# Performance work log

Hardware: AMD Instinct MI355X
Metric: run time of the kernel (lower is better)

Reference implementation:

```python
import jax, jax.numpy as jnp
import numpy as np

B, C, H, W = 32, 64, 56, 56
REPN, NK, SMALL = 50, 17, 3   # repN=64-int(64*0.23), nk=ceil(51/3)
GROUPS = 4                     # N_rep
EPS = 1e-5


def _build_index_mats():
    """Reduce the fallback's python scatter-add loops to exact linear maps.
    For flat position p=r*NK+j the roll shifts depend only on p%3, so each
    shift class s gets a (REPN,NK) count matrix over source nk-slots."""
    rng = np.random.RandomState(123)
    ghost = np.sort(rng.choice(C, C - REPN, replace=False))
    rep = np.array(sorted(set(range(C)) - set(ghost.tolist())), np.int32)
    Mh = np.zeros((3, REPN, NK), np.int32)
    Mv = np.zeros((3, REPN, NK), np.int32)
    Mid = np.zeros((REPN, NK), np.int32)
    for _ in range(GROUPS):
        for r in range(REPN):
            perm = rng.permutation(NK)
            for p in range(NK):
                Mh[(r * NK + p) % 3, r, perm[p]] += 1
        for r in range(REPN):
            perm = rng.permutation(NK)
            for p in range(NK):
                Mv[(r * NK + p) % 3, r, perm[p]] += 1
        kk = rng.randint(0, NK, REPN)
        for r in range(REPN):
            Mid[r, kk[r]] += 1
    return ghost.astype(np.int32), rep, Mh, Mv, Mid


def setup_inputs() -> dict:
    key = jax.random.key(0)
    k1, k2, k3 = jax.random.split(key, 3)
    ghost, rep, Mh, Mv, Mid = _build_index_mats()
    return {
        "inputs": jax.random.normal(k1, (B, C, H, W), jnp.float32),
        "w0": jax.random.normal(k2, (REPN * NK, 1, SMALL, SMALL), jnp.float32) * 0.1,
        "w1": jax.random.normal(k3, (REPN * NK, 1, SMALL, SMALL), jnp.float32) * 0.1,
        "Mh": jnp.asarray(Mh), "Mv": jnp.asarray(Mv), "Mid": jnp.asarray(Mid),
        "ghost_idx": jnp.asarray(ghost), "rep_idx": jnp.asarray(rep),
    }


def _bn(x):
    # BatchNorm2d in training mode, affine weight=1 / bias=0 (init values)
    m = x.mean(axis=(0, 2, 3), keepdims=True)
    v = x.var(axis=(0, 2, 3), keepdims=True)
    return (x - m) / jnp.sqrt(v + EPS)


def reference(inputs, w0, w1, Mh, Mv, Mid, ghost_idx, rep_idx):
    rep_in = inputs[:, rep_idx]      # (B, REPN, H, W)
    ghost_in = inputs[:, ghost_idx]  # (B, ghostN, H, W)

    def conv(w):  # depthwise-grouped conv: groups=REPN, each 1->NK channels
        return jax.lax.conv_general_dilated(
            rep_in, w, window_strides=(1, 1), padding=((2, 2), (2, 2)),
            dimension_numbers=('NCHW', 'OIHW', 'NCHW'),
            feature_group_count=REPN)

    out = conv(w0) + conv(w1)                       # (B, REPN*NK, H+2, W+2)
    xv = out.reshape(B, REPN, NK, H + 2, W + 2)

    Mhf, Mvf, Midf = (m.astype(xv.dtype) for m in (Mh, Mv, Mid))
    sh1, sw1 = (0, 1, 2), (0, 2, 1)   # lora1: shifts (i%3, 2i%3)
    sh2, sw2 = (0, 2, 1), (0, 1, 2)   # lora2: shifts (2i%3, i%3)

    lora1 = sum(jnp.roll(jnp.einsum('rk,brkhw->brhw', Mhf[s], xv),
                         (sh1[s], sw1[s]), axis=(2, 3)) for s in range(3))
    lora2 = sum(jnp.roll(jnp.einsum('rk,brkhw->brhw', Mvf[s], xv),
                         (sh2[s], sw2[s]), axis=(2, 3)) for s in range(3))
    small = jnp.einsum('rk,brkhw->brhw', Midf, xv)

    # center-crop back to (H, W): dh = dw = 1
    lora1 = lora1[:, :, 1:1 + H, 1:1 + W]
    lora2 = lora2[:, :, 1:1 + H, 1:1 + W]
    small = small[:, :, 1:1 + H, 1:1 + W]

    x = _bn(lora1) + _bn(lora2) + _bn(small) + rep_in
    return jnp.concatenate([x, ghost_in], axis=1)   # (B, C, H, W)
```

## Files before the change

kernel.cpp:

```cpp
#include <hip/hip_runtime.h>

#define Bn 32
#define Cn 64
#define Hn 56
#define Wn 56
#define REPN 50
#define NKn 17
#define HWn (Hn*Wn)
#define NSTATf 100352.0f
#define EPSf 1e-5f

#define GCNT_OFF 0
#define GSUM_OFF 1600
#define INIT_BYTES 8000
#define PART_OFF 4096

#define SEGH 7
#define NTASK 112
#define GRID_FUSED 1024

__device__ __forceinline__ void block_weff(int r, int tid,
        const float* __restrict__ w0, const float* __restrict__ w1,
        const int* __restrict__ Mh, const int* __restrict__ Mv,
        const int* __restrict__ Mid, float* __restrict__ swk)
{
    if (tid >= 0 && tid < 63) {
        int t = tid / 9, ij = tid - t*9;
        const int* M = (t < 3) ? (Mh + (t*REPN + r)*NKn)
                     : (t < 6) ? (Mv + ((t-3)*REPN + r)*NKn)
                               : (Mid + r*NKn);
        float acc = 0.f;
        #pragma unroll
        for (int k = 0; k < NKn; ++k)
            acc += (float)M[k] * (w0[(r*NKn + k)*9 + ij] + w1[(r*NKn + k)*9 + ij]);
        swk[t*9 + ij] = acc;
    }
}

__device__ __forceinline__ void load_row8c(const float* __restrict__ ch, int row, int q,
                                           float* __restrict__ X, float& c55)
{
    bool rv = (row >= 0) && (row < Hn);
    int rc = rv ? row : 0;
    const float* rp = ch + rc*Wn;
    float4 c0 = *(const float4*)(rp + (q ? 4*q - 4 : 0));
    float4 c1 = *(const float4*)(rp + 4*q);
    int ox = (4*q + 4 <= 55) ? 4*q + 4 : 55;
    float cx = rp[ox];
    float mr = rv ? 1.f : 0.f;
    float m0 = (rv && q > 0)  ? 1.f : 0.f;
    float mx = (rv && q < 13) ? 1.f : 0.f;
    X[0]=c0.y*m0; X[1]=c0.z*m0; X[2]=c0.w*m0;
    X[3]=c1.x*mr; X[4]=c1.y*mr; X[5]=c1.z*mr; X[6]=c1.w*mr;
    X[7]=cx*mx;
    c55 = (q == 0) ? rp[55]*mr : 0.f;
}

template <typename F>
__device__ __forceinline__ void conv_walk3(const float* __restrict__ ch,
        const float (&wk)[63], int tid, F emit)
{
    if (tid >= NTASK) return;
    int seg = tid / 14;
    int q   = tid - seg*14;
    int h0  = seg * SEGH;
    bool top = (seg == 0);

    float W[6][8], C[6], T[8];
    {
        float dummy;
        if (top) load_row8c(ch, 55, q, T, dummy);
    }
    #pragma unroll
    for (int k = 0; k < 6; ++k)
        load_row8c(ch, h0 - 3 + k, q, W[k], C[k]);

    #pragma unroll
    for (int s = 0; s < SEGH; ++s) {
        int h = h0 + s;
        float Wn8[8], Cn1;
        load_row8c(ch, h + 3, q, Wn8, Cn1);

        float l1[4], l2[4], sm[4];
        #pragma unroll
        for (int p = 0; p < 4; ++p) { l1[p]=0.f; l2[p]=0.f; sm[p]=0.f; }
        #pragma unroll
        for (int i = 0; i < 3; ++i)
            #pragma unroll
            for (int j = 0; j < 3; ++j) {
                int ij = i*3 + j;
                float wh0 = wk[ij],    wh1 = wk[9+ij],  wh2 = wk[18+ij];
                float wv0 = wk[27+ij], wv1 = wk[36+ij], wv2 = wk[45+ij];
                float wid = wk[54+ij];
                #pragma unroll
                for (int p = 0; p < 4; ++p) {
                    float a  = W[2+i][p+2+j];
                    l1[p] = fmaf(a, wh0, l1[p]);
                    l2[p] = fmaf(a, wv0, l2[p]);
                    sm[p] = fmaf(a, wid, sm[p]);
                    float bA = W[1+i][p+j];
                    l1[p] = fmaf(bA, wh1, l1[p]);
                    l2[p] = fmaf(bA, wv2, l2[p]);
                    float bB = W[i][p+1+j];
                    l1[p] = fmaf(bB, wh2, l1[p]);
                    l2[p] = fmaf(bB, wv1, l2[p]);
                }
            }
        if (q == 0) {
            #pragma unroll
            for (int i = 0; i < 3; ++i) {
                l1[0] = fmaf(C[1+i], wk[9+3*i],  l1[0]);
                l2[0] = fmaf(C[1+i], wk[45+3*i], l2[0]);
            }
        }
        if (s == 0 && top) {
            #pragma unroll
            for (int j = 0; j < 3; ++j)
                #pragma unroll
                for (int p = 0; p < 4; ++p) {
                    l1[p] = fmaf(T[p+1+j], wk[18+j], l1[p]);
                    l2[p] = fmaf(T[p+1+j], wk[36+j], l2[p]);
                }
        }
        float res[4] = {W[3][3], W[3][4], W[3][5], W[3][6]};
        emit(h, q, l1, l2, sm, res);

        #pragma unroll
        for (int k = 0; k < 5; ++k) {
            #pragma unroll
            for (int x = 0; x < 8; ++x) W[k][x] = W[k+1][x];
            C[k] = C[k+1];
        }
        #pragma unroll
        for (int x = 0; x < 8; ++x) W[5][x] = Wn8[x];
        C[5] = Cn1;
    }
}

__device__ __forceinline__ void conv_walk1(const float* __restrict__ ch,
        const float (&cw0)[9], const float (&cwA)[9], const float (&cwB)[9],
        float Kc, int tid, float* __restrict__ dst)
{
    if (tid >= NTASK) return;
    int seg = tid / 14;
    int q   = tid - seg*14;
    int h0  = seg * SEGH;
    bool top = (seg == 0);

    float W[6][8], C[6], T[8];
    {
        float dummy;
        if (top) load_row8c(ch, 55, q, T, dummy);
    }
    #pragma unroll
    for (int k = 0; k < 6; ++k)
        load_row8c(ch, h0 - 3 + k, q, W[k], C[k]);

    #pragma unroll
    for (int s = 0; s < SEGH; ++s) {
        int h = h0 + s;
        float Wn8[8], Cn1;
        load_row8c(ch, h + 3, q, Wn8, Cn1);

        float acc[4];
        #pragma unroll
        for (int p = 0; p < 4; ++p) acc[p] = 0.f;
        #pragma unroll
        for (int i = 0; i < 3; ++i)
            #pragma unroll
            for (int j = 0; j < 3; ++j) {
                int ij = i*3 + j;
                float w0c = cw0[ij], wAc = cwA[ij], wBc = cwB[ij];
                #pragma unroll
                for (int p = 0; p < 4; ++p) {
                    acc[p] = fmaf(W[2+i][p+2+j], w0c, acc[p]);
                    acc[p] = fmaf(W[1+i][p+j],   wAc, acc[p]);
                    acc[p] = fmaf(W[i][p+1+j],   wBc, acc[p]);
                }
            }
        if (q == 0) {
            #pragma unroll
            for (int i = 0; i < 3; ++i)
                acc[0] = fmaf(C[1+i], cwA[3*i], acc[0]);
        }
        if (s == 0 && top) {
            #pragma unroll
            for (int j = 0; j < 3; ++j)
                #pragma unroll
                for (int p = 0; p < 4; ++p)
                    acc[p] = fmaf(T[p+1+j], cwB[j], acc[p]);
        }
        float4 o;
        o.x = acc[0] - Kc + W[3][3];
        o.y = acc[1] - Kc + W[3][4];
        o.z = acc[2] - Kc + W[3][5];
        o.w = acc[3] - Kc + W[3][6];
        *(float4*)(dst + h*Wn + 4*q) = o;

        #pragma unroll
        for (int k = 0; k < 5; ++k) {
            #pragma unroll
            for (int x = 0; x < 8; ++x) W[k][x] = W[k+1][x];
            C[k] = C[k+1];
        }
        #pragma unroll
        for (int x = 0; x < 8; ++x) W[5][x] = Wn8[x];
        C[5] = Cn1;
    }
}

__device__ __forceinline__ void stats_and_arrive(const float* __restrict__ ch,
        const float* __restrict__ swk, int r, int tid,
        float* __restrict__ ws, float (*red)[6])
{
    float wk[63];
    #pragma unroll
    for (int i = 0; i < 63; ++i) wk[i] = swk[i];

    float s1=0.f,q1=0.f,s2=0.f,q2=0.f,s3=0.f,q3=0.f;
    conv_walk3(ch, wk, tid,
        [&](int h, int q, float* l1, float* l2, float* sm, float* res) {
            (void)h; (void)q; (void)res;
            #pragma unroll
            for (int p = 0; p < 4; ++p) {
                s1 += l1[p]; q1 += l1[p]*l1[p];
                s2 += l2[p]; q2 += l2[p]*l2[p];
                s3 += sm[p]; q3 += sm[p]*sm[p];
            }
        });
    {
        float vals[6] = {s1,q1,s2,q2,s3,q3};
        int lane = tid & 63, wave = tid >> 6;
        #pragma unroll
        for (int x = 0; x < 6; ++x) {
            float y = vals[x];
            for (int o = 32; o; o >>= 1) y += __shfl_down(y, o, 64);
            if (lane == 0) red[wave][x] = y;
        }
    }
    __syncthreads();
    if (tid < 6) {
        atomicAdd(ws + GSUM_OFF + r*8 + tid, red[0][tid] + red[1][tid]);
        __threadfence();
    }
    __syncthreads();
    if (tid == 0)
        atomicAdd(((unsigned*)ws) + GCNT_OFF + r*32, 1u);
    __syncthreads();
}

__device__ __forceinline__ void wait_and_finalize(const float* __restrict__ ch,
        const float* __restrict__ swk, int r, int tid,
        float* __restrict__ ws, float* __restrict__ sred,
        float* __restrict__ dst)
{
    if (tid == 0) {
        unsigned* gc = ((unsigned*)ws) + GCNT_OFF + r*32;
        while (atomicAdd(gc, 0u) < (unsigned)Bn)
            __builtin_amdgcn_s_sleep(8);
    }
    __syncthreads();
    if (tid < 6) sred[tid] = atomicAdd(ws + GSUM_OFF + r*8 + tid, 0.f);
    __syncthreads();

    const float inv = 1.0f / NSTATf;
    float m1 = sred[0]*inv, v1 = sred[1]*inv - m1*m1;
    float m2 = sred[2]*inv, v2 = sred[3]*inv - m2*m2;
    float m3 = sred[4]*inv, v3 = sred[5]*inv - m3*m3;
    float r1 = rsqrtf(v1 + EPSf), r2 = rsqrtf(v2 + EPSf), r3 = rsqrtf(v3 + EPSf);
    float Kc = m1*r1 + m2*r2 + m3*r3;

    float cw0[9], cwA[9], cwB[9];
    #pragma unroll
    for (int ij = 0; ij < 9; ++ij) {
        cw0[ij] = r1*swk[ij]    + r2*swk[27+ij] + r3*swk[54+ij];
        cwA[ij] = r1*swk[9+ij]  + r2*swk[45+ij];
        cwB[ij] = r1*swk[18+ij] + r2*swk[36+ij];
    }
    conv_walk1(ch, cw0, cwA, cwB, Kc, tid, dst);
}

__global__ void __launch_bounds__(128) k_fused(const float* __restrict__ in,
        const float* __restrict__ w0, const float* __restrict__ w1,
        const int* __restrict__ Mh, const int* __restrict__ Mv,
        const int* __restrict__ Mid,
        const int* __restrict__ rep_idx, const int* __restrict__ ghost_idx,
        float* __restrict__ ws, float* __restrict__ out)
{
    int tid = threadIdx.x;
    int bid = blockIdx.x;
    int b   = bid >> 5;
    int pr  = bid & 31;
    int cA  = 2*pr, cB = 2*pr + 1;

    if (pr >= REPN/2) {
        #pragma unroll
        for (int it = 0; it < 2; ++it) {
            int c = cA + it;
            int cin = ghost_idx[c - REPN];
            const float4* s4 = (const float4*)(in + ((size_t)(b*Cn + cin))*HWn);
            float4* d4 = (float4*)(out + ((size_t)(b*Cn + c))*HWn);
            for (int i = tid; i < HWn/4; i += 128) d4[i] = s4[i];
        }
        return;
    }

    __shared__ float swkA[63], swkB[63];
    __shared__ float red[2][6];
    __shared__ float sredA[6], sredB[6];

    block_weff(cA, tid,      w0, w1, Mh, Mv, Mid, swkA);
    block_weff(cB, tid - 64, w0, w1, Mh, Mv, Mid, swkB);
    __syncthreads();

    const float* chA = in + ((size_t)(b*Cn + rep_idx[cA]))*HWn;
    const float* chB = in + ((size_t)(b*Cn + rep_idx[cB]))*HWn;

    stats_and_arrive(chA, swkA, cA, tid, ws, red);
    stats_and_arrive(chB, swkB, cB, tid, ws, red);

    float* dstA = out + ((size_t)(b*Cn + cA))*HWn;
    float* dstB = out + ((size_t)(b*Cn + cB))*HWn;
    wait_and_finalize(chA, swkA, cA, tid, ws, sredA, dstA);
    wait_and_finalize(chB, swkB, cB, tid, ws, sredB, dstB);
}

__global__ void __launch_bounds__(128) k_pass1(const float* __restrict__ in,
        const float* __restrict__ w0, const float* __restrict__ w1,
        const int* __restrict__ Mh, const int* __restrict__ Mv,
        const int* __restrict__ Mid,
        const int* __restrict__ rep_idx, float* __restrict__ ws)
{
    int bid = blockIdx.x;
    int r = bid % REPN;
    int b = bid / REPN;
    int tid = threadIdx.x;

    __shared__ float swk[63];
    __shared__ float red[2][6];

    block_weff(r, tid, w0, w1, Mh, Mv, Mid, swk);
    __syncthreads();
    float wk[63];
    #pragma unroll
    for (int i = 0; i < 63; ++i) wk[i] = swk[i];

    const float* ch = in + ((size_t)(b*Cn + rep_idx[r]))*HWn;

    float s1=0.f,q1=0.f,s2=0.f,q2=0.f,s3=0.f,q3=0.f;
    conv_walk3(ch, wk, tid,
        [&](int h, int q, float* l1, float* l2, float* sm, float* res) {
            (void)h; (void)q; (void)res;
            #pragma unroll
            for (int p = 0; p < 4; ++p) {
                s1 += l1[p]; q1 += l1[p]*l1[p];
                s2 += l2[p]; q2 += l2[p]*l2[p];
                s3 += sm[p]; q3 += sm[p]*sm[p];
            }
        });

    float vals[6] = {s1,q1,s2,q2,s3,q3};
    int lane = tid & 63, wave = tid >> 6;
    #pragma unroll
    for (int x = 0; x < 6; ++x) {
        float y = vals[x];
        for (int o = 32; o; o >>= 1) y += __shfl_down(y, o, 64);
        if (lane == 0) red[wave][x] = y;
    }
    __syncthreads();
    if (tid < 6)
        ws[PART_OFF + (tid*REPN + r)*Bn + b] = red[0][tid] + red[1][tid];
}

__global__ void __launch_bounds__(128) k_pass2(const float* __restrict__ in,
        const float* __restrict__ w0, const float* __restrict__ w1,
        const int* __restrict__ Mh, const int* __restrict__ Mv,
        const int* __restrict__ Mid,
        const int* __restrict__ rep_idx, const int* __restrict__ ghost_idx,
        const float* __restrict__ ws, float* __restrict__ out)
{
    int bid = blockIdx.x;
    int c = bid & 63;
    int b = bid >> 6;
    int tid = threadIdx.x;

    if (c >= REPN) {
        int cin = ghost_idx[c - REPN];
        const float4* s4 = (const float4*)(in + ((size_t)(b*Cn + cin))*HWn);
        float4* d4 = (float4*)(out + ((size_t)(b*Cn + c))*HWn);
        for (int i = tid; i < HWn/4; i += 128) d4[i] = s4[i];
        return;
    }
    int r = c;

    __shared__ float swk[63];
    __shared__ float sred[6];

    block_weff(r, tid, w0, w1, Mh, Mv, Mid, swk);
    if (tid >= 64 && tid < 70) {
        int x = tid - 64;
        const float* pp = ws + PART_OFF + (x*REPN + r)*Bn;
        float s = 0.f;
        #pragma unroll
        for (int i = 0; i < Bn; ++i) s += pp[i];
        sred[x] = s;
    }
    __syncthreads();

    const float inv = 1.0f / NSTATf;
    float m1 = sred[0]*inv, v1 = sred[1]*inv - m1*m1;
    float m2 = sred[2]*inv, v2 = sred[3]*inv - m2*m2;
    float m3 = sred[4]*inv, v3 = sred[5]*inv - m3*m3;
    float r1 = rsqrtf(v1 + EPSf), r2 = rsqrtf(v2 + EPSf), r3 = rsqrtf(v3 + EPSf);
    float Kc = m1*r1 + m2*r2 + m3*r3;

    float cw0[9], cwA[9], cwB[9];
    #pragma unroll
    for (int ij = 0; ij < 9; ++ij) {
        cw0[ij] = r1*swk[ij]    + r2*swk[27+ij] + r3*swk[54+ij];
        cwA[ij] = r1*swk[9+ij]  + r2*swk[45+ij];
        cwB[ij] = r1*swk[18+ij] + r2*swk[36+ij];
    }

    const float* ch = in + ((size_t)(b*Cn + rep_idx[r]))*HWn;
    float* dst = out + ((size_t)(b*Cn + c))*HWn;
    conv_walk1(ch, cw0, cwA, cwB, Kc, tid, dst);
}

extern "C" void kernel_launch(void* const* d_in, const int* in_sizes, int n_in,
                              void* d_out, int out_size, void* d_ws, size_t ws_size,
                              hipStream_t stream) {
    const float* in   = (const float*)d_in[0];
    const float* w0   = (const float*)d_in[1];
    const float* w1   = (const float*)d_in[2];
    const int*   Mh   = (const int*)d_in[3];
    const int*   Mv   = (const int*)d_in[4];
    const int*   Mid  = (const int*)d_in[5];
    const int*   ghost= (const int*)d_in[6];
    const int*   rep  = (const int*)d_in[7];
    float* out  = (float*)d_out;
    float* ws   = (float*)d_ws;

    int maxBlk = 0;
    hipError_t qerr = hipOccupancyMaxActiveBlocksPerMultiprocessor(
        &maxBlk, (const void*)k_fused, 128, 0);
    bool fused_ok = (qerr == hipSuccess) && (maxBlk >= 4);

    if (fused_ok) {
        hipError_t merr = hipMemsetAsync(ws, 0, INIT_BYTES, stream);
        if (merr == hipSuccess) {
            k_fused<<<GRID_FUSED, 128, 0, stream>>>(in, w0, w1, Mh, Mv, Mid,
                                                    rep, ghost, ws, out);
            return;
        }
    }
    k_pass1<<<REPN*Bn, 128, 0, stream>>>(in, w0, w1, Mh, Mv, Mid, rep, ws);
    k_pass2<<<Bn*Cn,   128, 0, stream>>>(in, w0, w1, Mh, Mv, Mid, rep, ghost, ws, out);
}
```

Before: 118.3 us.

## Cache conv branch outputs as bf16 in LDS instead of recomputing in finalize

During the statistics pass, each block now packs the three pre-normalization branch outputs (lora1, lora2, small) into bf16 planes in shared memory. After the grid-wide statistics wait, the finalize step reads these planes and applies the per-branch BN scales plus the residual, instead of rerunning the 3x3 convolution walk. This removes the second convolution pass over the input at the cost of about 37 KB of LDS per block, which may lower occupancy. Storing the intermediates in bf16 also introduces rounding error in the normalized outputs.

Result: no change. 118.3 us (+0.1%).

```diff
diff --git a/kernel.cpp b/kernel.cpp
--- a/kernel.cpp
+++ b/kernel.cpp
@@ -18,6 +18,18 @@
 #define SEGH 7
 #define NTASK 112
 #define GRID_FUSED 1024
+#define PLW (HWn/2)
+
+__device__ __forceinline__ unsigned bfpack2(float a, float b)
+{
+    unsigned ua = __float_as_uint(a);
+    unsigned ub = __float_as_uint(b);
+    ua += 0x7FFFu + ((ua >> 16) & 1u);
+    ub += 0x7FFFu + ((ub >> 16) & 1u);
+    return (ua >> 16) | (ub & 0xFFFF0000u);
+}
+__device__ __forceinline__ float bflo(unsigned u){ return __uint_as_float(u << 16); }
+__device__ __forceinline__ float bfhi(unsigned u){ return __uint_as_float(u & 0xFFFF0000u); }
 
 __device__ __forceinline__ void block_weff(int r, int tid,
         const float* __restrict__ w0, const float* __restrict__ w1,
@@ -211,7 +223,7 @@
 
 __device__ __forceinline__ void stats_and_arrive(const float* __restrict__ ch,
         const float* __restrict__ swk, int r, int tid,
-        float* __restrict__ ws, float (*red)[6])
+        float* __restrict__ ws, float (*red)[6], unsigned* __restrict__ pl)
 {
     float wk[63];
     #pragma unroll
@@ -220,13 +232,17 @@
     float s1=0.f,q1=0.f,s2=0.f,q2=0.f,s3=0.f,q3=0.f;
     conv_walk3(ch, wk, tid,
         [&](int h, int q, float* l1, float* l2, float* sm, float* res) {
-            (void)h; (void)q; (void)res;
+            (void)res;
             #pragma unroll
             for (int p = 0; p < 4; ++p) {
                 s1 += l1[p]; q1 += l1[p]*l1[p];
                 s2 += l2[p]; q2 += l2[p]*l2[p];
                 s3 += sm[p]; q3 += sm[p]*sm[p];
             }
+            int b2 = (h*Wn + 4*q) >> 1;
+            *(uint2*)&pl[0*PLW + b2] = make_uint2(bfpack2(l1[0],l1[1]), bfpack2(l1[2],l1[3]));
+            *(uint2*)&pl[1*PLW + b2] = make_uint2(bfpack2(l2[0],l2[1]), bfpack2(l2[2],l2[3]));
+            *(uint2*)&pl[2*PLW + b2] = make_uint2(bfpack2(sm[0],sm[1]), bfpack2(sm[2],sm[3]));
         });
     {
         float vals[6] = {s1,q1,s2,q2,s3,q3};
@@ -250,9 +266,8 @@
 }
 
 __device__ __forceinline__ void wait_and_finalize(const float* __restrict__ ch,
-        const float* __restrict__ swk, int r, int tid,
-        float* __restrict__ ws, float* __restrict__ sred,
-        float* __restrict__ dst)
+        int r, int tid, float* __restrict__ ws, float* __restrict__ sred,
+        const unsigned* __restrict__ pl, float* __restrict__ dst)
 {
     if (tid == 0) {
         unsigned* gc = ((unsigned*)ws) + GCNT_OFF + r*32;
@@ -270,14 +285,26 @@
     float r1 = rsqrtf(v1 + EPSf), r2 = rsqrtf(v2 + EPSf), r3 = rsqrtf(v3 + EPSf);
     float Kc = m1*r1 + m2*r2 + m3*r3;
 
-    float cw0[9], cwA[9], cwB[9];
-    #pragma unroll
-    for (int ij = 0; ij < 9; ++ij) {
-        cw0[ij] = r1*swk[ij]    + r2*swk[27+ij] + r3*swk[54+ij];
-        cwA[ij] = r1*swk[9+ij]  + r2*swk[45+ij];
-        cwB[ij] = r1*swk[18+ij] + r2*swk[36+ij];
-    }
-    conv_walk1(ch, cw0, cwA, cwB, Kc, tid, dst);
+    if (tid >= NTASK) return;
+    int seg = tid / 14;
+    int q   = tid - seg*14;
+    int h0  = seg * SEGH;
+
+    #pragma unroll
+    for (int s = 0; s < SEGH; ++s) {
+        int bi = (h0 + s)*Wn + 4*q;
+        int b2 = bi >> 1;
+        float4 res = *(const float4*)(ch + bi);
+        uint2 u1 = *(const uint2*)&pl[0*PLW + b2];
+        uint2 u2 = *(const uint2*)&pl[1*PLW + b2];
+        uint2 u3 = *(const uint2*)&pl[2*PLW + b2];
+        float4 o;
+        o.x = bflo(u1.x)*r1 + bflo(u2.x)*r2 + bflo(u3.x)*r3 - Kc + res.x;
+        o.y = bfhi(u1.x)*r1 + bfhi(u2.x)*r2 + bfhi(u3.x)*r3 - Kc + res.y;
+        o.z = bflo(u1.y)*r1 + bflo(u2.y)*r2 + bflo(u3.y)*r3 - Kc + res.z;
+        o.w = bfhi(u1.y)*r1 + bfhi(u2.y)*r2 + bfhi(u3.y)*r3 - Kc + res.w;
+        *(float4*)(dst + bi) = o;
+    }
 }
 
 __global__ void __launch_bounds__(128) k_fused(const float* __restrict__ in,
@@ -305,6 +332,7 @@
         return;
     }
 
+    __shared__ unsigned planes[2][3*PLW];
     __shared__ float swkA[63], swkB[63];
     __shared__ float red[2][6];
     __shared__ float sredA[6], sredB[6];
@@ -316,13 +344,13 @@
     const float* chA = in + ((size_t)(b*Cn + rep_idx[cA]))*HWn;
     const float* chB = in + ((size_t)(b*Cn + rep_idx[cB]))*HWn;
 
-    stats_and_arrive(chA, swkA, cA, tid, ws, red);
-    stats_and_arrive(chB, swkB, cB, tid, ws, red);
+    stats_and_arrive(chA, swkA, cA, tid, ws, red, planes[0]);
+    stats_and_arrive(chB, swkB, cB, tid, ws, red, planes[1]);
 
     float* dstA = out + ((size_t)(b*Cn + cA))*HWn;
     float* dstB = out + ((size_t)(b*Cn + cB))*HWn;
-    wait_and_finalize(chA, swkA, cA, tid, ws, sredA, dstA);
-    wait_and_finalize(chB, swkB, cB, tid, ws, sredB, dstB);
+    wait_and_finalize(chA, cA, tid, ws, sredA, planes[0], dstA);
+    wait_and_finalize(chB, cB, tid, ws, sredB, planes[1], dstB);
 }
 
 __global__ void __launch_bounds__(128) k_pass1(const float* __restrict__ in,
```
